# Kernel optimization log

Measured on AMD Instinct MI355X. Metric: run time of the kernel, lower is better.

The kernel has to match this reference:

```python
import jax, jax.numpy as jnp
import numpy as np


def setup_inputs() -> dict:
    key = jax.random.key(0)
    ka, kb = jax.random.split(key)
    a = jax.random.normal(ka, (16384, 3), dtype=jnp.float32)
    b = jax.random.normal(kb, (16384, 3), dtype=jnp.float32)
    return {"a": a, "b": b}


def reference(a, b):
    # Pairwise squared L2 via the expansion ||a-b||^2 = ||a||^2 + ||b||^2 - 2 a.b,
    # avoiding materializing the [N, M, D] diff tensor the torch code builds.
    a2 = jnp.sum(a * a, axis=-1)                      # [N]
    b2 = jnp.sum(b * b, axis=-1)                      # [M]
    cross = jnp.einsum("nd,md->nm", a, b)             # [N, M]
    d2 = a2[:, None] + b2[None, :] - 2.0 * cross       # [N, M]
    dist = jnp.sqrt(jnp.maximum(d2, 0.0))              # clamp for numerical safety
    min_dist = jnp.min(dist, axis=1)                   # [N] nearest-neighbor dist
    return jnp.sum(min_dist)
```

## Files before the change

kernel.cpp:

```cpp
#include <hip/hip_runtime.h>
#include <math.h>


#define NPTS 16384

typedef short s16x8 __attribute__((ext_vector_type(8)));
typedef unsigned short u16x8 __attribute__((ext_vector_type(8)));
typedef float f32x16 __attribute__((ext_vector_type(16)));

__device__ __forceinline__ unsigned short f2bf(float x) {
    unsigned u = __float_as_uint(x);
    u = u + 0x7FFFu + ((u >> 16) & 1u);
    return (unsigned short)(u >> 16);
}
__device__ __forceinline__ float bf2f(unsigned short h) {
    return __uint_as_float((unsigned)h << 16);
}

__global__ __launch_bounds__(256)
void cd_pair_kernel(const float* __restrict__ a,
                    const float* __restrict__ b,
                    unsigned int* __restrict__ gmin) {
    __shared__ u16x8 bpk8[1024];
    const int tid   = threadIdx.x;
    const int lane  = tid & 63;
    const int wave  = tid >> 6;
    const int col   = lane & 31;
    const int khalf = lane >> 5;

    const int bbase = blockIdx.y * 512;
    for (int jj = tid; jj < 512; jj += 256) {
        const int p = bbase + jj;
        const float x = b[3 * p + 0];
        const float y = b[3 * p + 1];
        const float z = b[3 * p + 2];
        const float n2 = fmaf(x, x, fmaf(y, y, z * z));
        const unsigned short hx = f2bf(x), hy = f2bf(y), hz = f2bf(z);
        const unsigned short thx = f2bf(-2.0f * bf2f(hx));
        const unsigned short thy = f2bf(-2.0f * bf2f(hy));
        const unsigned short thz = f2bf(-2.0f * bf2f(hz));
        const unsigned short tlx = f2bf(-2.0f * (x - bf2f(hx)));
        const unsigned short tly = f2bf(-2.0f * (y - bf2f(hy)));
        const unsigned short tlz = f2bf(-2.0f * (z - bf2f(hz)));
        const unsigned short n2h = f2bf(n2);
        const unsigned short n2l = f2bf(n2 - bf2f(n2h));
        const unsigned short one = f2bf(1.0f);
        const u16x8 v0 = {thx, thy, thz, tlx, tly, tlz, thx, thy};
        const u16x8 v1 = {thz, tlx, tly, tlz, one, one, n2h, n2l};
        bpk8[2 * jj + 0] = v0;
        bpk8[2 * jj + 1] = v1;
    }

    const int abase = blockIdx.x * 256 + wave * 64;
    s16x8 af0, af1;
    #pragma unroll
    for (int q = 0; q < 2; ++q) {
        const int row = abase + col + 32 * q;
        const float x = a[3 * row + 0];
        const float y = a[3 * row + 1];
        const float z = a[3 * row + 2];
        const float n2 = fmaf(x, x, fmaf(y, y, z * z));
        const unsigned short hx = f2bf(x), hy = f2bf(y), hz = f2bf(z);
        const unsigned short lx = f2bf(x - bf2f(hx));
        const unsigned short ly = f2bf(y - bf2f(hy));
        const unsigned short lz = f2bf(z - bf2f(hz));
        const unsigned short n2h = f2bf(n2);
        const unsigned short n2l = f2bf(n2 - bf2f(n2h));
        const unsigned short one = f2bf(1.0f);
        const s16x8 lo = {(short)hx, (short)hy, (short)hz, (short)hx,
                          (short)hy, (short)hz, (short)lx, (short)ly};
        const s16x8 hi = {(short)lz, (short)lx, (short)ly, (short)lz,
                          (short)n2h, (short)n2l, (short)one, (short)one};
        const s16x8 f = khalf ? hi : lo;
        if (q == 0) af0 = f; else af1 = f;
    }
    __syncthreads();

    f32x16 best0, best1, zero;
    #pragma unroll
    for (int r = 0; r < 16; ++r) {
        best0[r] = 3.4028235e38f; best1[r] = 3.4028235e38f; zero[r] = 0.0f;
    }

    const unsigned short* bp = (const unsigned short*)bpk8 + col * 16 + khalf * 8;
    #pragma unroll
    for (int t = 0; t < 16; t += 2) {
        const s16x8 b0 = *(const s16x8*)(bp + t * 512);
        const s16x8 b1 = *(const s16x8*)(bp + t * 512 + 512);
        const f32x16 c00 = __builtin_amdgcn_mfma_f32_32x32x16_bf16(b0, af0, zero, 0, 0, 0);
        const f32x16 c01 = __builtin_amdgcn_mfma_f32_32x32x16_bf16(b1, af0, zero, 0, 0, 0);
        const f32x16 c10 = __builtin_amdgcn_mfma_f32_32x32x16_bf16(b0, af1, zero, 0, 0, 0);
        const f32x16 c11 = __builtin_amdgcn_mfma_f32_32x32x16_bf16(b1, af1, zero, 0, 0, 0);
        #pragma unroll
        for (int r = 0; r < 16; ++r) {
            best0[r] = fminf(fminf(c00[r], c01[r]), best0[r]);
            best1[r] = fminf(fminf(c10[r], c11[r]), best1[r]);
        }
    }

    float m0 = best0[0], m1 = best1[0];
    #pragma unroll
    for (int r = 1; r < 16; ++r) {
        m0 = fminf(m0, best0[r]);
        m1 = fminf(m1, best1[r]);
    }
    m0 = fminf(m0, __shfl_xor(m0, 32, 64));
    m1 = fminf(m1, __shfl_xor(m1, 32, 64));
    m0 = fmaxf(m0, 0.0f);
    m1 = fmaxf(m1, 0.0f);

    if (lane < 32) {
        atomicMin(&gmin[abase + col],      __float_as_uint(m0));
        atomicMin(&gmin[abase + col + 32], __float_as_uint(m1));
    }
}

__global__ __launch_bounds__(1024)
void cd_reduce_kernel(const unsigned int* __restrict__ gmin,
                      float* __restrict__ out) {
    __shared__ float red[16];
    const int tid = threadIdx.x;
    const float4* g4 = (const float4*)gmin;

    float s = 0.0f;
    #pragma unroll
    for (int i = tid; i < NPTS / 4; i += 1024) {
        const float4 v = g4[i];
        s += sqrtf(v.x) + sqrtf(v.y) + sqrtf(v.z) + sqrtf(v.w);
    }
    for (int off = 32; off > 0; off >>= 1)
        s += __shfl_down(s, off, 64);
    if ((tid & 63) == 0) red[tid >> 6] = s;
    __syncthreads();
    if (tid == 0) {
        float t = 0.0f;
        #pragma unroll
        for (int w = 0; w < 16; ++w) t += red[w];
        out[0] = t;
    }
}

extern "C" void kernel_launch(void* const* d_in, const int* in_sizes, int n_in,
                              void* d_out, int out_size, void* d_ws, size_t ws_size,
                              hipStream_t stream) {
    const float* a = (const float*)d_in[0];
    const float* b = (const float*)d_in[1];
    float* out = (float*)d_out;
    unsigned int* gmin = (unsigned int*)d_ws;

    dim3 grid(NPTS / 256, NPTS / 512);
    cd_pair_kernel<<<grid, 256, 0, stream>>>(a, b, gmin);
    cd_reduce_kernel<<<1, 1024, 0, stream>>>(gmin, out);
}
```

Measured before the change: 72.64 us.

## Prepack bf16 operands in separate kernel and sweep B from global without atomics

Adds a pack kernel that converts a and b once into split-bf16 MFMA operand formats in workspace. The sweep kernel gives each block 32 rows of a, splits all of b across 8 waves that stream compact 16-byte records from global memory, and reduces the per-wave minima in shared memory before one plain store. This removes the redundant per-block conversions, the LDS staging and the global atomicMin traffic. In exchange it adds a kernel launch and a global/L2 read stream for b inside the inner loop.

New measurement: 70.88 us. -2.4%, faster.

```diff
diff --git a/kernel.cpp b/kernel.cpp
--- a/kernel.cpp
+++ b/kernel.cpp
@@ -5,7 +5,7 @@
 #define NPTS 16384
 
 typedef short s16x8 __attribute__((ext_vector_type(8)));
-typedef unsigned short u16x8 __attribute__((ext_vector_type(8)));
+typedef unsigned int u32x4 __attribute__((ext_vector_type(4)));
 typedef float f32x16 __attribute__((ext_vector_type(16)));
 
 __device__ __forceinline__ unsigned short f2bf(float x) {
@@ -16,24 +16,32 @@
 __device__ __forceinline__ float bf2f(unsigned short h) {
     return __uint_as_float((unsigned)h << 16);
 }
+__device__ __forceinline__ unsigned pk(unsigned short lo, unsigned short hi) {
+    return (unsigned)lo | ((unsigned)hi << 16);
+}
 
 __global__ __launch_bounds__(256)
-void cd_pair_kernel(const float* __restrict__ a,
+void cd_pack_kernel(const float* __restrict__ a,
                     const float* __restrict__ b,
-                    unsigned int* __restrict__ gmin) {
-    __shared__ u16x8 bpk8[1024];
-    const int tid   = threadIdx.x;
-    const int lane  = tid & 63;
-    const int wave  = tid >> 6;
-    const int col   = lane & 31;
-    const int khalf = lane >> 5;
-
-    const int bbase = blockIdx.y * 512;
-    for (int jj = tid; jj < 512; jj += 256) {
-        const int p = bbase + jj;
-        const float x = b[3 * p + 0];
-        const float y = b[3 * p + 1];
-        const float z = b[3 * p + 2];
+                    u32x4* __restrict__ aexp,
+                    u32x4* __restrict__ bcmp) {
+    const int i = blockIdx.x * 256 + threadIdx.x;
+    {
+        const float x = a[3 * i + 0], y = a[3 * i + 1], z = a[3 * i + 2];
+        const float n2 = fmaf(x, x, fmaf(y, y, z * z));
+        const unsigned short hx = f2bf(x), hy = f2bf(y), hz = f2bf(z);
+        const unsigned short lx = f2bf(x - bf2f(hx));
+        const unsigned short ly = f2bf(y - bf2f(hy));
+        const unsigned short lz = f2bf(z - bf2f(hz));
+        const unsigned short n2h = f2bf(n2), n2l = f2bf(n2 - bf2f(n2h));
+        const unsigned short one = 0x3F80u;
+        const u32x4 lo = { pk(hx, hy), pk(hz, hx), pk(hy, hz), pk(lx, ly) };
+        const u32x4 hi = { pk(lz, lx), pk(ly, lz), pk(n2h, n2l), pk(one, one) };
+        aexp[2 * i + 0] = lo;
+        aexp[2 * i + 1] = hi;
+    }
+    {
+        const float x = b[3 * i + 0], y = b[3 * i + 1], z = b[3 * i + 2];
         const float n2 = fmaf(x, x, fmaf(y, y, z * z));
         const unsigned short hx = f2bf(x), hy = f2bf(y), hz = f2bf(z);
         const unsigned short thx = f2bf(-2.0f * bf2f(hx));
@@ -42,81 +50,71 @@
         const unsigned short tlx = f2bf(-2.0f * (x - bf2f(hx)));
         const unsigned short tly = f2bf(-2.0f * (y - bf2f(hy)));
         const unsigned short tlz = f2bf(-2.0f * (z - bf2f(hz)));
-        const unsigned short n2h = f2bf(n2);
-        const unsigned short n2l = f2bf(n2 - bf2f(n2h));
-        const unsigned short one = f2bf(1.0f);
-        const u16x8 v0 = {thx, thy, thz, tlx, tly, tlz, thx, thy};
-        const u16x8 v1 = {thz, tlx, tly, tlz, one, one, n2h, n2l};
-        bpk8[2 * jj + 0] = v0;
-        bpk8[2 * jj + 1] = v1;
+        const unsigned short n2h = f2bf(n2), n2l = f2bf(n2 - bf2f(n2h));
+        bcmp[i] = (u32x4){ pk(thx, thy), pk(thz, tlx), pk(tly, tlz), pk(n2h, n2l) };
+    }
+}
+
+__global__ __launch_bounds__(512, 4)
+void cd_sweep_kernel(const u32x4* __restrict__ aexp,
+                     const u32x4* __restrict__ bcmp,
+                     float* __restrict__ gmin) {
+    __shared__ float red[8][32];
+    const int tid   = threadIdx.x;
+    const int lane  = tid & 63;
+    const int wave  = tid >> 6;
+    const int col   = lane & 31;
+    const int khalf = lane >> 5;
+
+    const u32x4 av = aexp[(blockIdx.x * 32 + col) * 2 + khalf];
+    const s16x8 af = __builtin_bit_cast(s16x8, av);
+
+    f32x16 best, zero;
+    #pragma unroll
+    for (int r = 0; r < 16; ++r) { best[r] = 3.4028235e38f; zero[r] = 0.0f; }
+
+    const unsigned Kone = 0x3F803F80u;
+    const u32x4* bp = bcmp + wave * 2048 + col;
+
+    #pragma unroll 2
+    for (int t = 0; t < 64; t += 2) {
+        const u32x4 d0 = bp[(t + 0) * 32];
+        const u32x4 d1 = bp[(t + 1) * 32];
+        u32x4 e0, e1;
+        e0[0] = khalf ? d0[1] : d0[0];
+        e0[1] = khalf ? d0[2] : d0[1];
+        e0[2] = khalf ? Kone  : d0[2];
+        e0[3] = khalf ? d0[3] : d0[0];
+        e1[0] = khalf ? d1[1] : d1[0];
+        e1[1] = khalf ? d1[2] : d1[1];
+        e1[2] = khalf ? Kone  : d1[2];
+        e1[3] = khalf ? d1[3] : d1[0];
+        const f32x16 c0 = __builtin_amdgcn_mfma_f32_32x32x16_bf16(
+            __builtin_bit_cast(s16x8, e0), af, zero, 0, 0, 0);
+        const f32x16 c1 = __builtin_amdgcn_mfma_f32_32x32x16_bf16(
+            __builtin_bit_cast(s16x8, e1), af, zero, 0, 0, 0);
+        #pragma unroll
+        for (int r = 0; r < 16; ++r)
+            best[r] = fminf(fminf(c0[r], c1[r]), best[r]);
     }
 
-    const int abase = blockIdx.x * 256 + wave * 64;
-    s16x8 af0, af1;
+    float m = best[0];
     #pragma unroll
-    for (int q = 0; q < 2; ++q) {
-        const int row = abase + col + 32 * q;
-        const float x = a[3 * row + 0];
-        const float y = a[3 * row + 1];
-        const float z = a[3 * row + 2];
-        const float n2 = fmaf(x, x, fmaf(y, y, z * z));
-        const unsigned short hx = f2bf(x), hy = f2bf(y), hz = f2bf(z);
-        const unsigned short lx = f2bf(x - bf2f(hx));
-        const unsigned short ly = f2bf(y - bf2f(hy));
-        const unsigned short lz = f2bf(z - bf2f(hz));
-        const unsigned short n2h = f2bf(n2);
-        const unsigned short n2l = f2bf(n2 - bf2f(n2h));
-        const unsigned short one = f2bf(1.0f);
-        const s16x8 lo = {(short)hx, (short)hy, (short)hz, (short)hx,
-                          (short)hy, (short)hz, (short)lx, (short)ly};
-        const s16x8 hi = {(short)lz, (short)lx, (short)ly, (short)lz,
-                          (short)n2h, (short)n2l, (short)one, (short)one};
-        const s16x8 f = khalf ? hi : lo;
-        if (q == 0) af0 = f; else af1 = f;
-    }
+    for (int r = 1; r < 16; ++r) m = fminf(m, best[r]);
+    m = fminf(m, __shfl_xor(m, 32, 64));
+
+    if (lane < 32) red[wave][col] = m;
     __syncthreads();
-
-    f32x16 best0, best1, zero;
-    #pragma unroll
-    for (int r = 0; r < 16; ++r) {
-        best0[r] = 3.4028235e38f; best1[r] = 3.4028235e38f; zero[r] = 0.0f;
-    }
-
-    const unsigned short* bp = (const unsigned short*)bpk8 + col * 16 + khalf * 8;
-    #pragma unroll
-    for (int t = 0; t < 16; t += 2) {
-        const s16x8 b0 = *(const s16x8*)(bp + t * 512);
-        const s16x8 b1 = *(const s16x8*)(bp + t * 512 + 512);
-        const f32x16 c00 = __builtin_amdgcn_mfma_f32_32x32x16_bf16(b0, af0, zero, 0, 0, 0);
-        const f32x16 c01 = __builtin_amdgcn_mfma_f32_32x32x16_bf16(b1, af0, zero, 0, 0, 0);
-        const f32x16 c10 = __builtin_amdgcn_mfma_f32_32x32x16_bf16(b0, af1, zero, 0, 0, 0);
-        const f32x16 c11 = __builtin_amdgcn_mfma_f32_32x32x16_bf16(b1, af1, zero, 0, 0, 0);
+    if (tid < 32) {
+        float v = red[0][tid];
         #pragma unroll
-        for (int r = 0; r < 16; ++r) {
-            best0[r] = fminf(fminf(c00[r], c01[r]), best0[r]);
-            best1[r] = fminf(fminf(c10[r], c11[r]), best1[r]);
-        }
-    }
-
-    float m0 = best0[0], m1 = best1[0];
-    #pragma unroll
-    for (int r = 1; r < 16; ++r) {
-        m0 = fminf(m0, best0[r]);
-        m1 = fminf(m1, best1[r]);
-    }
-    m0 = fminf(m0, __shfl_xor(m0, 32, 64));
-    m1 = fminf(m1, __shfl_xor(m1, 32, 64));
-    m0 = fmaxf(m0, 0.0f);
-    m1 = fmaxf(m1, 0.0f);
-
-    if (lane < 32) {
-        atomicMin(&gmin[abase + col],      __float_as_uint(m0));
-        atomicMin(&gmin[abase + col + 32], __float_as_uint(m1));
+        for (int w = 1; w < 8; ++w) v = fminf(v, red[w][tid]);
+        gmin[blockIdx.x * 32 + tid] = fmaxf(v, 0.0f);
     }
 }
 
 __global__ __launch_bounds__(1024)
-void cd_reduce_kernel(const unsigned int* __restrict__ gmin,
+void cd_reduce_kernel(const float* __restrict__ gmin,
                       float* __restrict__ out) {
     __shared__ float red[16];
     const int tid = threadIdx.x;
@@ -146,9 +144,12 @@
     const float* a = (const float*)d_in[0];
     const float* b = (const float*)d_in[1];
     float* out = (float*)d_out;
-    unsigned int* gmin = (unsigned int*)d_ws;
+    char* ws = (char*)d_ws;
+    u32x4* aexp = (u32x4*)(ws + 0);
+    u32x4* bcmp = (u32x4*)(ws + 512 * 1024);
+    float* gmin = (float*)(ws + 768 * 1024);
 
-    dim3 grid(NPTS / 256, NPTS / 512);
-    cd_pair_kernel<<<grid, 256, 0, stream>>>(a, b, gmin);
+    cd_pack_kernel<<<NPTS / 256, 256, 0, stream>>>(a, b, aexp, bcmp);
+    cd_sweep_kernel<<<NPTS / 32, 512, 0, stream>>>(aexp, bcmp, gmin);
     cd_reduce_kernel<<<1, 1024, 0, stream>>>(gmin, out);
 }
```
